# Kernel tuning notes

Hardware: AMD Instinct MI355X
Metric: run time of the kernel (lower is better)

Reference implementation:

```python
import jax, jax.numpy as jnp
import numpy as np

B, NV, NP, D, K = 8, 2048, 4096, 64, 8  # shapes per batch, vtx/pts counts, feat dim, num_interp
NEG = -1e9


def _unit(x):
    return x / jnp.clip(jnp.linalg.norm(x, axis=-1, keepdims=True), 1e-12)


def _gather(v, idx):
    # v: [B, N, C], idx: [B, Q, K] -> [B, Q, K, C]
    return jax.vmap(lambda a, i: a[i])(v, idx)


def setup_inputs() -> dict:
    key = jax.random.key(0)
    k1, k2, k3, k4, k5 = jax.random.split(key, 5)
    return {
        "vtx": jax.random.normal(k1, (B * NV, 3), jnp.float32),
        "pts": jax.random.normal(k2, (B * NP, 3), jnp.float32),
        "vtx_feature": jax.random.normal(k3, (B * NV, D), jnp.float32),
        "pts_feature": jax.random.normal(k4, (B * NP, D), jnp.float32),
        "vismask_logits": jax.random.normal(k5, (B * NV, 1), jnp.float32),
    }


def reference(vtx, pts, vtx_feature, pts_feature, vismask_logits):
    # --- per-batch min-max normalization of sigmoid(vismask) (serial loop in torch) ---
    vm = jax.nn.sigmoid(vismask_logits).reshape(B, NV, 1)
    vmin = vm.min(axis=1, keepdims=True)
    vmax = vm.max(axis=1, keepdims=True)
    vm = (vm - vmin) / (vmax - vmin)

    vtxb = vtx.reshape(B, NV, 3)
    ptsb = pts.reshape(B, NP, 3)
    vf = vtx_feature.reshape(B, NV, D)
    pf = pts_feature.reshape(B, NP, D)

    # --- cosine KNN: for each vtx, k nearest pts by cosine similarity ---
    sim = jnp.einsum('bnd,bmd->bnm', _unit(vf), _unit(pf))  # [B,NV,NP]
    _, idx = jax.lax.top_k(sim, K)                           # [B,NV,K]

    nbr_pts = _gather(ptsb, idx)                             # [B,NV,K,3]
    nbr_pf = _gather(pf, idx)                                # [B,NV,K,D]
    euclid = nbr_pts - vtxb[:, :, None, :]
    # raw (unnormalized) dot product, weighted by vismask of the query vertex
    fsim = jnp.sum(nbr_pf * vf[:, :, None, :], axis=-1, keepdims=True) * vm[:, :, None, :]
    # scatter_add over assign_index[0] == sum over the K grouped neighbors
    flow_init = jnp.sum(euclid * fsim, axis=2) / jnp.sum(fsim, axis=2)  # [B,NV,3]

    # --- interpolate flow at invisible vertices from visible ones (2nd cosine KNN) ---
    vis = vm >= 0.5                                          # [B,NV,1]
    vfn = _unit(vf)
    sim2 = jnp.einsum('bnd,bmd->bnm', vfn, vfn)              # [B,NV,NV]
    sim2 = jnp.where(vis[:, :, 0][:, None, :], sim2, NEG)    # keys restricted to visible vtx
    _, idx2 = jax.lax.top_k(sim2, K)                         # [B,NV,K]

    nbr_vf = _gather(vf, idx2)                               # [B,NV,K,D]
    nbr_flow = _gather(flow_init, idx2)                      # [B,NV,K,3]
    fsim2 = jnp.sum(nbr_vf * vf[:, :, None, :], axis=-1, keepdims=True)
    invis_flow = jnp.sum(nbr_flow * fsim2, axis=2) / jnp.sum(fsim2, axis=2)

    flow = jnp.where(vis, flow_init, invis_flow)             # flow_init[invis] = invis_flow
    l1_points = jnp.concatenate([flow, vm], axis=-1)         # [B,NV,4]
    return l1_points.reshape(B * NV, 4)
```

## Files before the change

### kernel.cpp

```cpp
#include <hip/hip_runtime.h>
#include <math.h>

#define BB 8
#define NVV 2048
#define NPP 4096
#define DD 64
#define NQ (BB * NVV)
#define QT (NQ / 16)

typedef __attribute__((ext_vector_type(8))) short short8;
typedef __attribute__((ext_vector_type(8))) unsigned short ushort8;
typedef __attribute__((ext_vector_type(4))) float f32x4;


__device__ __forceinline__ unsigned short bf16rn(float x) {
  unsigned u = __float_as_uint(x);
  return (unsigned short)((u + 0x7FFFu + ((u >> 16) & 1u)) >> 16);
}
__device__ __forceinline__ float bf2f(unsigned short h) {
  return __uint_as_float(((unsigned)h) << 16);
}

__device__ __forceinline__ void net8(unsigned* a, unsigned v) {
#pragma unroll
  for (int k = 0; k < 7; k++) {
    unsigned r;
    asm("v_med3_u32 %0, %1, %2, %3" : "=v"(r) : "v"(v), "v"(a[k]), "v"(a[k + 1]));
    a[k] = r;
  }
  a[7] = a[7] > v ? a[7] : v;
}

__device__ __forceinline__ void ins8(float* tv, int* ti, float v, int id) {
  bool c1 = v > tv[1], c2 = v > tv[2], c3 = v > tv[3];
  bool c4 = v > tv[4], c5 = v > tv[5], c6 = v > tv[6], c7 = v > tv[7];
  tv[0] = c1 ? tv[1] : v;                ti[0] = c1 ? ti[1] : id;
  tv[1] = c2 ? tv[2] : (c1 ? v : tv[1]); ti[1] = c2 ? ti[2] : (c1 ? id : ti[1]);
  tv[2] = c3 ? tv[3] : (c2 ? v : tv[2]); ti[2] = c3 ? ti[3] : (c2 ? id : ti[2]);
  tv[3] = c4 ? tv[4] : (c3 ? v : tv[3]); ti[3] = c4 ? ti[4] : (c3 ? id : ti[3]);
  tv[4] = c5 ? tv[5] : (c4 ? v : tv[4]); ti[4] = c5 ? ti[5] : (c4 ? id : ti[4]);
  tv[5] = c6 ? tv[6] : (c5 ? v : tv[5]); ti[5] = c6 ? ti[6] : (c5 ? id : ti[5]);
  tv[6] = c7 ? tv[7] : (c6 ? v : tv[6]); ti[6] = c7 ? ti[7] : (c6 ? id : ti[6]);
  tv[7] = c7 ? v : tv[7];                ti[7] = c7 ? id : ti[7];
}

__global__ __launch_bounds__(256) void k_prep(const float* __restrict__ logits,
                                              const float* __restrict__ vf,
                                              const float* __restrict__ pf,
                                              float* __restrict__ vm,
                                              float* __restrict__ inv_vf_s,
                                              float* __restrict__ inv_pf_s,
                                              unsigned short* __restrict__ vfh,
                                              unsigned short* __restrict__ vfl,
                                              unsigned short* __restrict__ pfh,
                                              unsigned short* __restrict__ pfl,
                                              float* __restrict__ out) {
  int bid = blockIdx.x, t = threadIdx.x;
  if (bid < BB) {
    int b = bid;
    __shared__ float smn[4], smx[4];
    float vals[8];
    float mn = 1e30f, mx = -1e30f;
#pragma unroll
    for (int i = 0; i < 8; i++) {
      float x = logits[b * NVV + t + i * 256];
      float s = 1.0f / (1.0f + expf(-x));
      vals[i] = s;
      mn = fminf(mn, s);
      mx = fmaxf(mx, s);
    }
    for (int o = 32; o; o >>= 1) {
      mn = fminf(mn, __shfl_xor(mn, o, 64));
      mx = fmaxf(mx, __shfl_xor(mx, o, 64));
    }
    int w = t >> 6;
    if ((t & 63) == 0) { smn[w] = mn; smx[w] = mx; }
    __syncthreads();
    mn = fminf(fminf(smn[0], smn[1]), fminf(smn[2], smn[3]));
    mx = fmaxf(fmaxf(smx[0], smx[1]), fmaxf(smx[2], smx[3]));
    float range = mx - mn;
#pragma unroll
    for (int i = 0; i < 8; i++) {
      float v = (vals[i] - mn) / range;
      int g = b * NVV + t + i * 256;
      vm[g] = v;
      out[g * 4 + 3] = v;
    }
  } else {
    int tile_g = (bid - BB) * 4 + (t >> 6);
    int lane = t & 63, c = lane & 15, quad = (lane >> 4) & 3;
    const float* src;
    unsigned short *dh, *dl;
    float* ginv;
    int tile;
    if (tile_g < QT) { tile = tile_g; src = vf; dh = vfh; dl = vfl; ginv = inv_vf_s; }
    else { tile = tile_g - QT; src = pf; dh = pfh; dl = pfl; ginv = inv_pf_s; }
    int row = tile * 16 + c;
    const float* rp = src + (size_t)row * DD + quad * 8;
    float4 a0 = *(const float4*)(rp);
    float4 b0 = *(const float4*)(rp + 4);
    float4 a1 = *(const float4*)(rp + 32);
    float4 b1 = *(const float4*)(rp + 36);
    float xs[16] = {a0.x, a0.y, a0.z, a0.w, b0.x, b0.y, b0.z, b0.w,
                    a1.x, a1.y, a1.z, a1.w, b1.x, b1.y, b1.z, b1.w};
    float ss = 0.f;
#pragma unroll
    for (int j = 0; j < 16; j++) ss = fmaf(xs[j], xs[j], ss);
    ss += __shfl_xor(ss, 16, 64);
    ss += __shfl_xor(ss, 32, 64);
    float inv = 1.0f / fmaxf(sqrtf(ss), 1e-12f);
    if (quad == 0) ginv[row] = 16384.0f * inv;
    ushort8 h, l;
    size_t s0 = (size_t)tile * 128 + lane;
#pragma unroll
    for (int j = 0; j < 8; j++) {
      float xn = xs[j] * inv;
      unsigned short hj = bf16rn(xn);
      h[j] = hj;
      l[j] = bf16rn(xn - bf2f(hj));
    }
    *(ushort8*)(dh + s0 * 8) = h;
    *(ushort8*)(dl + s0 * 8) = l;
#pragma unroll
    for (int j = 0; j < 8; j++) {
      float xn = xs[8 + j] * inv;
      unsigned short hj = bf16rn(xn);
      h[j] = hj;
      l[j] = bf16rn(xn - bf2f(hj));
    }
    *(ushort8*)(dh + (s0 + 64) * 8) = h;
    *(ushort8*)(dl + (s0 + 64) * 8) = l;
  }
}


#define LOADK(d0, d1, d2, d3, KH, KL, tile) do {            \
    size_t bo_ = (size_t)(tile) * 1024 + lane * 8;          \
    d0 = *(const short8*)((KH) + bo_);                      \
    d1 = *(const short8*)((KH) + bo_ + 512);                \
    d2 = *(const short8*)((KL) + bo_);                      \
    d3 = *(const short8*)((KL) + bo_ + 512);                \
  } while (0)

#define MFMA6(c_, h0_, h1_, l0_, l1_) do {                                  \
    c_ = __builtin_amdgcn_mfma_f32_16x16x32_bf16(h0_, qh0, c_, 0, 0, 0);    \
    c_ = __builtin_amdgcn_mfma_f32_16x16x32_bf16(h1_, qh1, c_, 0, 0, 0);    \
    c_ = __builtin_amdgcn_mfma_f32_16x16x32_bf16(h0_, ql0, c_, 0, 0, 0);    \
    c_ = __builtin_amdgcn_mfma_f32_16x16x32_bf16(h1_, ql1, c_, 0, 0, 0);    \
    c_ = __builtin_amdgcn_mfma_f32_16x16x32_bf16(l0_, qh0, c_, 0, 0, 0);    \
    c_ = __builtin_amdgcn_mfma_f32_16x16x32_bf16(l1_, qh1, c_, 0, 0, 0);    \
  } while (0)

#define COMP1(h0_, h1_, l0_, l1_, b16_) do {                                \
    f32x4 c_ = {0.f, 0.f, 0.f, 0.f};                                        \
    MFMA6(c_, h0_, h1_, l0_, l1_);                                          \
    unsigned u0_ = (unsigned)fmaxf(fmaf(c_[0], 520000.0f, 520000.0f), 0.0f);\
    net8(tvA, (u0_ << 12) | (unsigned)((b16_) + 0));                        \
    unsigned u1_ = (unsigned)fmaxf(fmaf(c_[1], 520000.0f, 520000.0f), 0.0f);\
    net8(tvA, (u1_ << 12) | (unsigned)((b16_) + 1));                        \
    unsigned u2_ = (unsigned)fmaxf(fmaf(c_[2], 520000.0f, 520000.0f), 0.0f);\
    net8(tvB, (u2_ << 12) | (unsigned)((b16_) + 2));                        \
    unsigned u3_ = (unsigned)fmaxf(fmaf(c_[3], 520000.0f, 520000.0f), 0.0f);\
    net8(tvB, (u3_ << 12) | (unsigned)((b16_) + 3));                        \
  } while (0)

#define COMP2(h0_, h1_, l0_, l1_, b16_, mp_) do {                           \
    float4 mv_ = *(const float4*)(mp_);                                     \
    f32x4 c_ = {0.f, 0.f, 0.f, 0.f};                                        \
    MFMA6(c_, h0_, h1_, l0_, l1_);                                          \
    unsigned u0_ = (unsigned)fmaxf(fmaf(c_[0], 520000.0f, 520000.0f), 0.0f);\
    unsigned p0_ = (u0_ << 12) | (unsigned)((b16_) + 0);                    \
    net8(tvA, (mv_.x >= 0.5f) ? p0_ : 0u);                                  \
    unsigned u1_ = (unsigned)fmaxf(fmaf(c_[1], 520000.0f, 520000.0f), 0.0f);\
    unsigned p1_ = (u1_ << 12) | (unsigned)((b16_) + 1);                    \
    net8(tvA, (mv_.y >= 0.5f) ? p1_ : 0u);                                  \
    unsigned u2_ = (unsigned)fmaxf(fmaf(c_[2], 520000.0f, 520000.0f), 0.0f);\
    unsigned p2_ = (u2_ << 12) | (unsigned)((b16_) + 2);                    \
    net8(tvB, (mv_.z >= 0.5f) ? p2_ : 0u);                                  \
    unsigned u3_ = (unsigned)fmaxf(fmaf(c_[3], 520000.0f, 520000.0f), 0.0f);\
    unsigned p3_ = (u3_ << 12) | (unsigned)((b16_) + 3);                    \
    net8(tvB, (mv_.w >= 0.5f) ? p3_ : 0u);                                  \
  } while (0)

__global__ __launch_bounds__(256)
void k_knn(const unsigned short* __restrict__ vfh, const unsigned short* __restrict__ vfl,
           const unsigned short* __restrict__ pfh, const unsigned short* __restrict__ pfl,
           const float* __restrict__ vm,
           unsigned* __restrict__ pc1, unsigned* __restrict__ pc2) {
  __shared__ unsigned mg[2][2][16][8];

  int p = blockIdx.x;
  int xcd = p & 7, j = p >> 3;
  int qt_g = xcd * 128 + j;
  int batch = xcd;
  int w = (int)threadIdx.x >> 6;
  int ck = w >> 1, hf = w & 1;
  int lane = threadIdx.x & 63, col = lane & 15, quad = lane >> 4;

  size_t ab = (size_t)qt_g * 1024 + lane * 8;
  short8 qh0 = *(const short8*)(vfh + ab);
  short8 qh1 = *(const short8*)(vfh + ab + 512);
  short8 ql0 = *(const short8*)(vfl + ab);
  short8 ql1 = *(const short8*)(vfl + ab + 512);
  asm volatile("" : "+a"(qh0), "+a"(qh1), "+a"(ql0), "+a"(ql1));

  unsigned tvA[8], tvB[8];

#pragma unroll
  for (int k = 0; k < 8; k++) { tvA[k] = 0u; tvB[k] = 0u; }
  {
    int bt0 = batch * 256 + ck * 128 + hf * 64;
    int tb16 = (ck * 128 + hf * 64) * 16 + quad * 4;
    short8 ah0, ah1, al0, al1, bh0, bh1, bl0, bl1;
    LOADK(ah0, ah1, al0, al1, pfh, pfl, bt0);
#pragma unroll 1
    for (int kt = 0; kt < 62; kt += 2) {
      LOADK(bh0, bh1, bl0, bl1, pfh, pfl, bt0 + kt + 1);
      COMP1(ah0, ah1, al0, al1, tb16 + kt * 16);
      LOADK(ah0, ah1, al0, al1, pfh, pfl, bt0 + kt + 2);
      COMP1(bh0, bh1, bl0, bl1, tb16 + (kt + 1) * 16);
    }
    LOADK(bh0, bh1, bl0, bl1, pfh, pfl, bt0 + 63);
    COMP1(ah0, ah1, al0, al1, tb16 + 62 * 16);
    COMP1(bh0, bh1, bl0, bl1, tb16 + 63 * 16);
  }
#pragma unroll
  for (int k = 0; k < 8; k++) net8(tvA, tvB[k]);
#pragma unroll
  for (int m = 16; m <= 32; m <<= 1) {
    unsigned ov[8];
#pragma unroll
    for (int k = 0; k < 8; k++) ov[k] = (unsigned)__shfl_xor((int)tvA[k], m, 64);
#pragma unroll
    for (int k = 7; k >= 0; k--) net8(tvA, ov[k]);
  }
  if (hf == 1 && quad == 0) {
#pragma unroll
    for (int k = 0; k < 8; k++) mg[0][ck][col][k] = tvA[k];
  }
  __syncthreads();
  if (hf == 0 && quad == 0) {
#pragma unroll
    for (int k = 0; k < 8; k++) net8(tvA, mg[0][ck][col][k]);
    int q = qt_g * 16 + col;
#pragma unroll
    for (int k = 0; k < 8; k++)
      pc1[(size_t)(ck * 8 + k) * NQ + q] = tvA[k];
  }

#pragma unroll
  for (int k = 0; k < 8; k++) { tvA[k] = 0u; tvB[k] = 0u; }
  {
    const float* mask = vm + batch * NVV;
    int bt0 = batch * 128 + ck * 64 + hf * 32;
    int tbase = ck * 64 + hf * 32;
    int tb16 = tbase * 16 + quad * 4;
    const float* mp0 = mask + tbase * 16 + quad * 4;
    short8 ah0, ah1, al0, al1, bh0, bh1, bl0, bl1;
    LOADK(ah0, ah1, al0, al1, vfh, vfl, bt0);
#pragma unroll 1
    for (int kt = 0; kt < 30; kt += 2) {
      LOADK(bh0, bh1, bl0, bl1, vfh, vfl, bt0 + kt + 1);
      COMP2(ah0, ah1, al0, al1, tb16 + kt * 16, mp0 + kt * 16);
      LOADK(ah0, ah1, al0, al1, vfh, vfl, bt0 + kt + 2);
      COMP2(bh0, bh1, bl0, bl1, tb16 + (kt + 1) * 16, mp0 + (kt + 1) * 16);
    }
    LOADK(bh0, bh1, bl0, bl1, vfh, vfl, bt0 + 31);
    COMP2(ah0, ah1, al0, al1, tb16 + 30 * 16, mp0 + 30 * 16);
    COMP2(bh0, bh1, bl0, bl1, tb16 + 31 * 16, mp0 + 31 * 16);
  }
#pragma unroll
  for (int k = 0; k < 8; k++) net8(tvA, tvB[k]);
#pragma unroll
  for (int m = 16; m <= 32; m <<= 1) {
    unsigned ov[8];
#pragma unroll
    for (int k = 0; k < 8; k++) ov[k] = (unsigned)__shfl_xor((int)tvA[k], m, 64);
#pragma unroll
    for (int k = 7; k >= 0; k--) net8(tvA, ov[k]);
  }
  if (hf == 1 && quad == 0) {
#pragma unroll
    for (int k = 0; k < 8; k++) mg[1][ck][col][k] = tvA[k];
  }
  __syncthreads();
  if (hf == 0 && quad == 0) {
#pragma unroll
    for (int k = 0; k < 8; k++) net8(tvA, mg[1][ck][col][k]);
    int q = qt_g * 16 + col;
#pragma unroll
    for (int k = 0; k < 8; k++)
      pc2[(size_t)(ck * 8 + k) * NQ + q] = tvA[k];
  }
}

__device__ __forceinline__ float dot64(const float4* __restrict__ a,
                                       const float4* __restrict__ b) {
  float a0 = 0.f, a1 = 0.f, a2 = 0.f, a3 = 0.f;
#pragma unroll
  for (int c = 0; c < 16; c++) {
    float4 x = a[c], y = b[c];
    a0 = fmaf(x.x, y.x, a0);
    a1 = fmaf(x.y, y.y, a1);
    a2 = fmaf(x.z, y.z, a2);
    a3 = fmaf(x.w, y.w, a3);
  }
  return (a0 + a1) + (a2 + a3);
}

__global__ __launch_bounds__(256) void k_merge_flow(const unsigned* __restrict__ pc,
                                                    const float* __restrict__ vf,
                                                    const float* __restrict__ pf,
                                                    const float* __restrict__ pts,
                                                    const float* __restrict__ vtx,
                                                    const float* __restrict__ inv_pf_s,
                                                    float* __restrict__ flow_ws,
                                                    float* __restrict__ out) {
  int T = blockIdx.x * 256 + threadIdx.x;
  int q = T >> 4, c = T & 15, batch = q >> 11;
  const float4* qp = (const float4*)(vf + (size_t)q * DD);
  float tv[8];
  int ti[8];
#pragma unroll
  for (int k = 0; k < 8; k++) { tv[k] = -3.0e38f; ti[k] = 0; }
  {
    unsigned pk = pc[(size_t)c * NQ + q];
    int id = (int)(pk & 0xFFFu);
    int prow = batch * NPP + id;
    float s = dot64(qp, (const float4*)(pf + (size_t)prow * DD)) *
              inv_pf_s[prow] * 6.103515625e-5f;
    ins8(tv, ti, s, id);
  }
#pragma unroll
  for (int m = 1; m <= 8; m <<= 1) {
    float ov[8];
    int oi[8];
#pragma unroll
    for (int k = 0; k < 8; k++) {
      ov[k] = __shfl_xor(tv[k], m, 64);
      oi[k] = __shfl_xor(ti[k], m, 64);
    }
#pragma unroll
    for (int k = 7; k >= 0; k--)
      if (ov[k] > tv[0]) ins8(tv, ti, ov[k], oi[k]);
  }
  int id = ti[0];
  float sv = tv[0];
#pragma unroll
  for (int k = 1; k < 8; k++) {
    id = (c == k) ? ti[k] : id;
    sv = (c == k) ? tv[k] : sv;
  }

  float ax = 0.f, ay = 0.f, az = 0.f, den = 0.f;
  if (c < 8) {
    int prow = batch * NPP + id;
    float w = sv * 16384.0f / inv_pf_s[prow];
    ax = (pts[prow * 3 + 0] - vtx[q * 3 + 0]) * w;
    ay = (pts[prow * 3 + 1] - vtx[q * 3 + 1]) * w;
    az = (pts[prow * 3 + 2] - vtx[q * 3 + 2]) * w;
    den = w;
  }
#pragma unroll
  for (int m = 1; m <= 8; m <<= 1) {
    ax += __shfl_xor(ax, m, 64);
    ay += __shfl_xor(ay, m, 64);
    az += __shfl_xor(az, m, 64);
    den += __shfl_xor(den, m, 64);
  }
  if (c == 0) {
    float fx = ax / den, fy = ay / den, fz = az / den;
    flow_ws[q * 4 + 0] = fx;
    flow_ws[q * 4 + 1] = fy;
    flow_ws[q * 4 + 2] = fz;
    out[q * 4 + 0] = fx;
    out[q * 4 + 1] = fy;
    out[q * 4 + 2] = fz;
  }
}

__global__ __launch_bounds__(256) void k_merge_final(const unsigned* __restrict__ pc,
                                                     const float* __restrict__ vf,
                                                     const float* __restrict__ vm,
                                                     const float* __restrict__ inv_vf_s,
                                                     const float* __restrict__ flow_ws,
                                                     float* __restrict__ out) {
  int T = blockIdx.x * 256 + threadIdx.x;
  int q = T >> 4, c = T & 15, batch = q >> 11;
  if (vm[q] >= 0.5f) return;
  const float4* qp = (const float4*)(vf + (size_t)q * DD);
  float tv[8];
  int ti[8];
#pragma unroll
  for (int k = 0; k < 8; k++) { tv[k] = -3.0e38f; ti[k] = 0; }
  {
    unsigned pk = pc[(size_t)c * NQ + q];
    if (pk > 0xFFFu) {
      int id = (int)(pk & 0xFFFu);
      int krow = batch * NVV + id;
      float s = dot64(qp, (const float4*)(vf + (size_t)krow * DD)) *
                inv_vf_s[krow] * 6.103515625e-5f;
      ins8(tv, ti, s, id);
    }
  }
#pragma unroll
  for (int m = 1; m <= 8; m <<= 1) {
    float ov[8];
    int oi[8];
#pragma unroll
    for (int k = 0; k < 8; k++) {
      ov[k] = __shfl_xor(tv[k], m, 64);
      oi[k] = __shfl_xor(ti[k], m, 64);
    }
#pragma unroll
    for (int k = 7; k >= 0; k--)
      if (ov[k] > tv[0]) ins8(tv, ti, ov[k], oi[k]);
  }
  int id = ti[0];
  float sv = tv[0];
#pragma unroll
  for (int k = 1; k < 8; k++) {
    id = (c == k) ? ti[k] : id;
    sv = (c == k) ? tv[k] : sv;
  }

  float ax = 0.f, ay = 0.f, az = 0.f, den = 0.f;
  if (c < 8) {
    int krow = batch * NVV + id;
    float w = sv * 16384.0f / inv_vf_s[krow];
    ax = flow_ws[krow * 4 + 0] * w;
    ay = flow_ws[krow * 4 + 1] * w;
    az = flow_ws[krow * 4 + 2] * w;
    den = w;
  }
#pragma unroll
  for (int m = 1; m <= 8; m <<= 1) {
    ax += __shfl_xor(ax, m, 64);
    ay += __shfl_xor(ay, m, 64);
    az += __shfl_xor(az, m, 64);
    den += __shfl_xor(den, m, 64);
  }
  if (c == 0) {
    out[q * 4 + 0] = ax / den;
    out[q * 4 + 1] = ay / den;
    out[q * 4 + 2] = az / den;
  }
}

extern "C" void kernel_launch(void* const* d_in, const int* in_sizes, int n_in,
                              void* d_out, int out_size, void* d_ws, size_t ws_size,
                              hipStream_t stream) {
  const float* vtx = (const float*)d_in[0];
  const float* pts = (const float*)d_in[1];
  const float* vf = (const float*)d_in[2];
  const float* pf = (const float*)d_in[3];
  const float* lg = (const float*)d_in[4];
  float* out = (float*)d_out;
  float* ws = (float*)d_ws;

  float* vm = ws;
  float* inv_vf_s = ws + 16384;
  float* inv_pf_s = ws + 32768;
  float* flow = ws + 65536;
  unsigned* pc1 = (unsigned*)(ws + 131072);
  unsigned* pc2 = (unsigned*)(ws + 393216);
  unsigned short* vfh = (unsigned short*)(ws + 655360);
  unsigned short* vfl = (unsigned short*)(ws + 1179648);
  unsigned short* pfh = (unsigned short*)(ws + 1703936);
  unsigned short* pfl = (unsigned short*)(ws + 2752512);

  k_prep<<<BB + 768, 256, 0, stream>>>(lg, vf, pf, vm, inv_vf_s, inv_pf_s,
                                       vfh, vfl, pfh, pfl, out);
  k_knn<<<1024, 256, 0, stream>>>(vfh, vfl, pfh, pfl, vm, pc1, pc2);
  k_merge_flow<<<NQ * 16 / 256, 256, 0, stream>>>(pc1, vf, pf, pts, vtx,
                                                  inv_pf_s, flow, out);
  k_merge_final<<<NQ * 16 / 256, 256, 0, stream>>>(pc2, vf, vm, inv_vf_s, flow, out);
}
```

Baseline: 174.7 us.

## Replace shuffle-merge top-8 with rank counting and remap blocks across XCDs

```diff
diff --git a/kernel.cpp b/kernel.cpp
--- a/kernel.cpp
+++ b/kernel.cpp
@@ -29,19 +29,6 @@
     a[k] = r;
   }
   a[7] = a[7] > v ? a[7] : v;
-}
-
-__device__ __forceinline__ void ins8(float* tv, int* ti, float v, int id) {
-  bool c1 = v > tv[1], c2 = v > tv[2], c3 = v > tv[3];
-  bool c4 = v > tv[4], c5 = v > tv[5], c6 = v > tv[6], c7 = v > tv[7];
-  tv[0] = c1 ? tv[1] : v;                ti[0] = c1 ? ti[1] : id;
-  tv[1] = c2 ? tv[2] : (c1 ? v : tv[1]); ti[1] = c2 ? ti[2] : (c1 ? id : ti[1]);
-  tv[2] = c3 ? tv[3] : (c2 ? v : tv[2]); ti[2] = c3 ? ti[3] : (c2 ? id : ti[2]);
-  tv[3] = c4 ? tv[4] : (c3 ? v : tv[3]); ti[3] = c4 ? ti[4] : (c3 ? id : ti[3]);
-  tv[4] = c5 ? tv[5] : (c4 ? v : tv[4]); ti[4] = c5 ? ti[5] : (c4 ? id : ti[4]);
-  tv[5] = c6 ? tv[6] : (c5 ? v : tv[5]); ti[5] = c6 ? ti[6] : (c5 ? id : ti[5]);
-  tv[6] = c7 ? tv[7] : (c6 ? v : tv[6]); ti[6] = c7 ? ti[7] : (c6 ? id : ti[6]);
-  tv[7] = c7 ? v : tv[7];                ti[7] = c7 ? id : ti[7];
 }
 
 __global__ __launch_bounds__(256) void k_prep(const float* __restrict__ logits,
@@ -308,6 +295,11 @@
   return (a0 + a1) + (a2 + a3);
 }
 
+__device__ __forceinline__ unsigned fkey(float s) {
+  unsigned u = __float_as_uint(s);
+  return ((int)u < 0) ? ~u : (u | 0x80000000u);
+}
+
 __global__ __launch_bounds__(256) void k_merge_flow(const unsigned* __restrict__ pc,
                                                     const float* __restrict__ vf,
                                                     const float* __restrict__ pf,
@@ -316,51 +308,35 @@
                                                     const float* __restrict__ inv_pf_s,
                                                     float* __restrict__ flow_ws,
                                                     float* __restrict__ out) {
-  int T = blockIdx.x * 256 + threadIdx.x;
+  int p = blockIdx.x;
+  int xcd = p & 7, jj = p >> 3;
+  int lb = xcd * 128 + jj;
+  int T = lb * 256 + (int)threadIdx.x;
   int q = T >> 4, c = T & 15, batch = q >> 11;
+  int lane = (int)threadIdx.x & 63;
+  int base = lane & 48;
+
+  unsigned pk = pc[(size_t)c * NQ + q];
+  int id = (int)(pk & 0xFFFu);
+  int prow = batch * NPP + id;
   const float4* qp = (const float4*)(vf + (size_t)q * DD);
-  float tv[8];
-  int ti[8];
-#pragma unroll
-  for (int k = 0; k < 8; k++) { tv[k] = -3.0e38f; ti[k] = 0; }
-  {
-    unsigned pk = pc[(size_t)c * NQ + q];
-    int id = (int)(pk & 0xFFFu);
-    int prow = batch * NPP + id;
-    float s = dot64(qp, (const float4*)(pf + (size_t)prow * DD)) *
-              inv_pf_s[prow] * 6.103515625e-5f;
-    ins8(tv, ti, s, id);
-  }
-#pragma unroll
-  for (int m = 1; m <= 8; m <<= 1) {
-    float ov[8];
-    int oi[8];
-#pragma unroll
-    for (int k = 0; k < 8; k++) {
-      ov[k] = __shfl_xor(tv[k], m, 64);
-      oi[k] = __shfl_xor(ti[k], m, 64);
-    }
-#pragma unroll
-    for (int k = 7; k >= 0; k--)
-      if (ov[k] > tv[0]) ins8(tv, ti, ov[k], oi[k]);
-  }
-  int id = ti[0];
-  float sv = tv[0];
-#pragma unroll
-  for (int k = 1; k < 8; k++) {
-    id = (c == k) ? ti[k] : id;
-    sv = (c == k) ? tv[k] : sv;
-  }
-
-  float ax = 0.f, ay = 0.f, az = 0.f, den = 0.f;
-  if (c < 8) {
-    int prow = batch * NPP + id;
-    float w = sv * 16384.0f / inv_pf_s[prow];
-    ax = (pts[prow * 3 + 0] - vtx[q * 3 + 0]) * w;
-    ay = (pts[prow * 3 + 1] - vtx[q * 3 + 1]) * w;
-    az = (pts[prow * 3 + 2] - vtx[q * 3 + 2]) * w;
-    den = w;
-  }
+  float dot = dot64(qp, (const float4*)(pf + (size_t)prow * DD));
+  float s = dot * inv_pf_s[prow];
+  unsigned kb = fkey(s);
+
+  int rank = 0;
+#pragma unroll
+  for (int i = 0; i < 16; i++) {
+    unsigned ok = (unsigned)__shfl((int)kb, base + i, 64);
+    int oid = __shfl(id, base + i, 64);
+    rank += (ok > kb || (ok == kb && oid > id)) ? 1 : 0;
+  }
+  float wgt = (rank < 8) ? dot : 0.0f;
+
+  float ax = (pts[prow * 3 + 0] - vtx[q * 3 + 0]) * wgt;
+  float ay = (pts[prow * 3 + 1] - vtx[q * 3 + 1]) * wgt;
+  float az = (pts[prow * 3 + 2] - vtx[q * 3 + 2]) * wgt;
+  float den = wgt;
 #pragma unroll
   for (int m = 1; m <= 8; m <<= 1) {
     ax += __shfl_xor(ax, m, 64);
@@ -385,54 +361,37 @@
                                                      const float* __restrict__ inv_vf_s,
                                                      const float* __restrict__ flow_ws,
                                                      float* __restrict__ out) {
-  int T = blockIdx.x * 256 + threadIdx.x;
+  int p = blockIdx.x;
+  int xcd = p & 7, jj = p >> 3;
+  int lb = xcd * 128 + jj;
+  int T = lb * 256 + (int)threadIdx.x;
   int q = T >> 4, c = T & 15, batch = q >> 11;
   if (vm[q] >= 0.5f) return;
+  int lane = (int)threadIdx.x & 63;
+  int base = lane & 48;
+
+  unsigned pk = pc[(size_t)c * NQ + q];
+  bool valid = pk > 0xFFFu;
+  int id = (int)(pk & 0xFFFu);
+  int krow = batch * NVV + id;
   const float4* qp = (const float4*)(vf + (size_t)q * DD);
-  float tv[8];
-  int ti[8];
-#pragma unroll
-  for (int k = 0; k < 8; k++) { tv[k] = -3.0e38f; ti[k] = 0; }
-  {
-    unsigned pk = pc[(size_t)c * NQ + q];
-    if (pk > 0xFFFu) {
-      int id = (int)(pk & 0xFFFu);
-      int krow = batch * NVV + id;
-      float s = dot64(qp, (const float4*)(vf + (size_t)krow * DD)) *
-                inv_vf_s[krow] * 6.103515625e-5f;
-      ins8(tv, ti, s, id);
-    }
-  }
-#pragma unroll
-  for (int m = 1; m <= 8; m <<= 1) {
-    float ov[8];
-    int oi[8];
-#pragma unroll
-    for (int k = 0; k < 8; k++) {
-      ov[k] = __shfl_xor(tv[k], m, 64);
-      oi[k] = __shfl_xor(ti[k], m, 64);
-    }
-#pragma unroll
-    for (int k = 7; k >= 0; k--)
-      if (ov[k] > tv[0]) ins8(tv, ti, ov[k], oi[k]);
-  }
-  int id = ti[0];
-  float sv = tv[0];
-#pragma unroll
-  for (int k = 1; k < 8; k++) {
-    id = (c == k) ? ti[k] : id;
-    sv = (c == k) ? tv[k] : sv;
-  }
-
-  float ax = 0.f, ay = 0.f, az = 0.f, den = 0.f;
-  if (c < 8) {
-    int krow = batch * NVV + id;
-    float w = sv * 16384.0f / inv_vf_s[krow];
-    ax = flow_ws[krow * 4 + 0] * w;
-    ay = flow_ws[krow * 4 + 1] * w;
-    az = flow_ws[krow * 4 + 2] * w;
-    den = w;
-  }
+  float dot = dot64(qp, (const float4*)(vf + (size_t)krow * DD));
+  float s = dot * inv_vf_s[krow];
+  unsigned kb = valid ? fkey(s) : 0u;
+
+  int rank = 0;
+#pragma unroll
+  for (int i = 0; i < 16; i++) {
+    unsigned ok = (unsigned)__shfl((int)kb, base + i, 64);
+    int oid = __shfl(id, base + i, 64);
+    rank += (ok > kb || (ok == kb && oid > id)) ? 1 : 0;
+  }
+  float wgt = (valid && rank < 8) ? dot : 0.0f;
+
+  float ax = flow_ws[krow * 4 + 0] * wgt;
+  float ay = flow_ws[krow * 4 + 1] * wgt;
+  float az = flow_ws[krow * 4 + 2] * wgt;
+  float den = wgt;
 #pragma unroll
   for (int m = 1; m <= 8; m <<= 1) {
     ax += __shfl_xor(ax, m, 64);
```

Result: faster. 169.7 us (-2.8%).
